# Optimization experiments

Hardware: AMD Instinct MI355X
Metric: run time of the kernel (lower is better)

## Reference

```python
import jax, jax.numpy as jnp
import numpy as np

B, S, E, H, D = 8, 1024, 1024, 16, 64
LN_EPS = 1e-5


def setup_inputs() -> dict:
    key = jax.random.key(0)
    ks = jax.random.split(key, 8)
    scale = 1.0 / np.sqrt(E)
    return {
        "query": jax.random.normal(ks[0], (B, S, E), jnp.float32),
        "key": jax.random.normal(ks[1], (B, S, E), jnp.float32),
        "value": jax.random.normal(ks[2], (B, S, E), jnp.float32),
        "self_attn_mask": jax.random.randint(ks[3], (B, S, S), 0, 2) == 1,
        "Wq": jax.random.normal(ks[4], (E, H * D), jnp.float32) * scale,
        "Wk": jax.random.normal(ks[5], (E, H * D), jnp.float32) * scale,
        "Wv": jax.random.normal(ks[6], (E, H * D), jnp.float32) * scale,
        "Wo": jax.random.normal(ks[7], (H * D, E), jnp.float32) * scale,
        "ln_gamma": jnp.ones((E,), jnp.float32),
        "ln_beta": jnp.zeros((E,), jnp.float32),
    }


def reference(query, key, value, self_attn_mask, Wq, Wk, Wv, Wo, ln_gamma, ln_beta):
    identity = query
    # project and split heads: [B, S, E] -> [B, H, S, D]
    q = (query @ Wq).reshape(B, S, H, D).transpose(0, 2, 1, 3)
    k = (key @ Wk).reshape(B, S, H, D).transpose(0, 2, 1, 3)
    v = (value @ Wv).reshape(B, S, H, D).transpose(0, 2, 1, 3)
    # scaled dot-product scores in fp32, additive mask fill -1e9
    score = jnp.einsum("bhsd,bhtd->bhst", q, k).astype(jnp.float32) / np.sqrt(D)
    score = jnp.where(self_attn_mask[:, None, :, :], jnp.float32(-1e9), score)
    attn = jax.nn.softmax(score, axis=-1)
    degree = jnp.einsum("bhst,bhtd->bhsd", attn, v)  # [B, H, S, D]
    degree = degree.transpose(0, 2, 1, 3).reshape(B, S, H * D)
    out = degree @ Wo + identity
    # LayerNorm over last dim
    mu = jnp.mean(out, axis=-1, keepdims=True)
    var = jnp.var(out, axis=-1, keepdims=True)
    out = (out - mu) * jax.lax.rsqrt(var + LN_EPS) * ln_gamma + ln_beta
    return out
```

## Files before the change

### kernel.cpp

```cpp
#include <hip/hip_runtime.h>
#include <hip/hip_bf16.h>
#include <cstdint>
#include <cstddef>

typedef __attribute__((ext_vector_type(8))) short bf16x8;
typedef __attribute__((ext_vector_type(8))) unsigned short ushort8;
typedef __attribute__((ext_vector_type(4))) unsigned short ushort4v;
typedef __attribute__((ext_vector_type(4))) float f32x4;

#define B_ 8
#define S_ 1024
#define E_ 1024
#define H_ 16
#define D_ 64
#define NW_ (S_ / 64)

__device__ __forceinline__ unsigned short f2bf(float f) {
    union { float fp; unsigned int u; } v; v.fp = f;
    unsigned int u = v.u;
    return (unsigned short)((u + 0x7fffu + ((u >> 16) & 1u)) >> 16);
}

__device__ __forceinline__ float fexp2(float x) {
    return __builtin_amdgcn_exp2f(x);
}

__device__ __forceinline__ unsigned cvt_pk_bf16(float lo, float hi) {
    unsigned r;
    asm("v_cvt_pk_bf16_f32 %0, %1, %2" : "=v"(r) : "v"(lo), "v"(hi));
    return r;
}

__device__ __forceinline__ void gload16(const void* g, void* l) {
    __builtin_amdgcn_global_load_lds((__attribute__((address_space(1))) void*)g,
                                     (__attribute__((address_space(3))) void*)l,
                                     16, 0, 0);
}

__global__ __launch_bounds__(256) void f32_to_bf16(const float* __restrict__ in,
                                                   unsigned short* __restrict__ out,
                                                   int n8) {
    int i = blockIdx.x * 256 + threadIdx.x;
    const int stride = gridDim.x * 256;
    for (; i < n8; i += stride) {
        float4 f0 = ((const float4*)in)[i * 2];
        float4 f1 = ((const float4*)in)[i * 2 + 1];
        union { unsigned u[4]; ushort8 v; } o;
        o.u[0] = cvt_pk_bf16(f0.x, f0.y);
        o.u[1] = cvt_pk_bf16(f0.z, f0.w);
        o.u[2] = cvt_pk_bf16(f1.x, f1.y);
        o.u[3] = cvt_pk_bf16(f1.z, f1.w);
        ((ushort8*)out)[i] = o.v;
    }
}

__global__ __launch_bounds__(256) void wtrans4(const float* __restrict__ W0,
                                               const float* __restrict__ W1,
                                               const float* __restrict__ W2,
                                               const float* __restrict__ W3,
                                               unsigned short* __restrict__ T0,
                                               unsigned short* __restrict__ T1,
                                               unsigned short* __restrict__ T2,
                                               unsigned short* __restrict__ T3) {
    const float* W = (blockIdx.z == 0) ? W0 : (blockIdx.z == 1) ? W1 : (blockIdx.z == 2) ? W2 : W3;
    unsigned short* Wt = (blockIdx.z == 0) ? T0 : (blockIdx.z == 1) ? T1 : (blockIdx.z == 2) ? T2 : T3;
    __shared__ float tile[32][33];
    const int k0 = blockIdx.y * 32, n0 = blockIdx.x * 32;
    const int tx = threadIdx.x & 31, ty = threadIdx.x >> 5;
#pragma unroll
    for (int i = ty; i < 32; i += 8)
        tile[i][tx] = W[(size_t)(k0 + i) * E_ + n0 + tx];
    __syncthreads();
#pragma unroll
    for (int i = ty; i < 32; i += 8)
        Wt[(size_t)(n0 + i) * E_ + k0 + tx] = f2bf(tile[tx][i]);
}

__global__ void detect_kernel(const unsigned int* __restrict__ m, int* __restrict__ flag) {
    unsigned int bad = 0;
    for (int i = threadIdx.x; i < 4096; i += 64) bad |= (m[i] > 1u) ? 1u : 0u;
    unsigned long long anybad = __ballot(bad != 0u);
    if (threadIdx.x == 0) *flag = (anybad == 0ull) ? 1 : 0;
}

__global__ __launch_bounds__(256) void pack_mask(const void* __restrict__ maskp,
                                                 const int* __restrict__ flagp,
                                                 unsigned long long* __restrict__ mbits) {
    const int mask32 = *flagp;
    const int lane = threadIdx.x & 63;
    const int gw = blockIdx.x * 4 + (threadIdx.x >> 6);
    const int nwaves = gridDim.x * 4;
    const int totw = B_ * S_ * NW_;
    for (int w = gw; w < totw; w += nwaves) {
        bool m;
        if (mask32) m = ((const int*)maskp)[(size_t)w * 64 + lane] != 0;
        else        m = ((const unsigned char*)maskp)[(size_t)w * 64 + lane] != 0;
        unsigned long long bits = __ballot(m);
        if (lane == 0) mbits[w] = bits;
    }
}

template <int EPI>
__global__ __launch_bounds__(256) void gemm_bt(const unsigned short* __restrict__ A,
                                               const unsigned short* __restrict__ Bt,
                                               void* __restrict__ Cp,
                                               const float* __restrict__ resid,
                                               float cscale) {
    __shared__ unsigned short As[128 * 64];
    __shared__ unsigned short Bs[128 * 64];
    const int t = threadIdx.x;
    const int lane = t & 63, w = t >> 6;
    const int wr = w >> 1, wc = w & 1;
    const int l15 = lane & 15, l4 = lane >> 4;
    const int m0 = blockIdx.x * 128, n0 = blockIdx.y * 128;

    const int lr = lane >> 3, lc = lane & 7;
    const int csrc = (lc ^ lr) * 8;
    const unsigned short* Ag[4];
    const unsigned short* Bg[4];
#pragma unroll
    for (int g = 0; g < 4; ++g) {
        Ag[g] = A + (size_t)(m0 + w * 32 + g * 8 + lr) * E_ + csrc;
        Bg[g] = Bt + (size_t)(n0 + w * 32 + g * 8 + lr) * E_ + csrc;
    }
    unsigned short* Al = &As[w * 32 * 64];
    unsigned short* Bl = &Bs[w * 32 * 64];

    f32x4 acc[4][4];
#pragma unroll
    for (int i = 0; i < 4; ++i)
#pragma unroll
        for (int j = 0; j < 4; ++j) acc[i][j] = (f32x4){0.f, 0.f, 0.f, 0.f};

    const int r7 = (l15 & 7) << 4;
    const char* AsB = (const char*)As;
    const char* BsB = (const char*)Bs;

    for (int kt = 0; kt < E_; kt += 64) {
#pragma unroll
        for (int g = 0; g < 4; ++g) {
            gload16(Ag[g] + kt, Al + g * 512);
            gload16(Bg[g] + kt, Bl + g * 512);
        }
        __syncthreads();
#pragma unroll
        for (int kk = 0; kk < 2; ++kk) {
            bf16x8 af[4], bfv[4];
#pragma unroll
            for (int mi = 0; mi < 4; ++mi)
                af[mi] = *(const bf16x8*)(AsB + (size_t)(wr * 64 + mi * 16 + l15) * 128 +
                                          ((((kk * 4 + l4) << 4)) ^ r7));
#pragma unroll
            for (int ni = 0; ni < 4; ++ni)
                bfv[ni] = *(const bf16x8*)(BsB + (size_t)(wc * 64 + ni * 16 + l15) * 128 +
                                           ((((kk * 4 + l4) << 4)) ^ r7));
#pragma unroll
            for (int mi = 0; mi < 4; ++mi)
#pragma unroll
                for (int ni = 0; ni < 4; ++ni)
                    acc[mi][ni] = __builtin_amdgcn_mfma_f32_16x16x32_bf16(af[mi], bfv[ni],
                                                                          acc[mi][ni], 0, 0, 0);
        }
        __syncthreads();
    }
#pragma unroll
    for (int mi = 0; mi < 4; ++mi) {
#pragma unroll
        for (int ni = 0; ni < 4; ++ni) {
#pragma unroll
            for (int r = 0; r < 4; ++r) {
                const int m = m0 + wr * 64 + mi * 16 + l4 * 4 + r;
                const int n = n0 + wc * 64 + ni * 16 + l15;
                const float v = acc[mi][ni][r];
                if (EPI == 0) {
                    const int b = m >> 10, s = m & 1023, h = n >> 6, d = n & 63;
                    ((unsigned short*)Cp)[(((size_t)b * H_ + h) * S_ + s) * D_ + d] = f2bf(v * cscale);
                } else if (EPI == 2) {
                    const int b = m >> 10, s = m & 1023, h = n >> 6, d = n & 63;
                    ((unsigned short*)Cp)[(((size_t)b * H_ + h) * D_ + d) * S_ + s] = f2bf(v);
                } else {
                    const size_t idx = (size_t)m * E_ + n;
                    ((float*)Cp)[idx] = v + resid[idx];
                }
            }
        }
    }
}

__global__ __launch_bounds__(256) void attn_kernel(const unsigned short* __restrict__ Qh,
                                                   const unsigned short* __restrict__ Kh,
                                                   const unsigned short* __restrict__ Vt,
                                                   const unsigned long long* __restrict__ mbits,
                                                   unsigned short* __restrict__ degree) {
    __shared__ unsigned short Ks[64 * 64];
    __shared__ unsigned short Vs[64 * 64];
    __shared__ unsigned short Ps[4 * 16 * 64];
    const int t = threadIdx.x;
    const int lane = t & 63, w = t >> 6;
    const int l15 = lane & 15, l4 = lane >> 4;
    const int i = blockIdx.x;
    const int L = (i & 7) * 256 + (i >> 3);
    const int bh = L >> 4, b = bh >> 4, h = bh & 15;
    const int q0 = (L & 15) * 64;
    const int myq = q0 + w * 16 + l15;

    const unsigned long long* mrow = mbits + ((size_t)b * S_ + myq) * NW_;

    bf16x8 qf[2];
    {
        const unsigned short* qptr = Qh + ((size_t)bh * S_ + myq) * D_ + l4 * 8;
        qf[0] = *(const bf16x8*)qptr;
        qf[1] = *(const bf16x8*)(qptr + 32);
    }
    f32x4 O[4];
#pragma unroll
    for (int idx = 0; idx < 4; ++idx) O[idx] = (f32x4){0.f, 0.f, 0.f, 0.f};
    float mrun = -3e38f, lrun = 0.f;

    const int srow = t >> 2, sch = (t & 3) * 2;
    const int ssw = (srow & 7) << 4;
    char* KsB = (char*)Ks;
    char* VsB = (char*)Vs;
    char* PsB = (char*)Ps + w * 2048;
    const int psw = (l15 & 7) << 4;

    const unsigned short* kgb = Kh + ((size_t)bh * S_ + srow) * D_ + sch * 8;
    const unsigned short* vgb = Vt + ((size_t)bh * D_ + srow) * S_ + sch * 8;

    ushort8 kp0 = *(const ushort8*)kgb;
    ushort8 kp1 = *(const ushort8*)(kgb + 8);
    ushort8 vp0 = *(const ushort8*)vgb;
    ushort8 vp1 = *(const ushort8*)(vgb + 8);

    for (int jt = 0; jt < S_; jt += 64) {
        const unsigned long long mw = mrow[jt >> 6];
        *(ushort8*)(KsB + srow * 128 + ((sch * 16) ^ ssw)) = kp0;
        *(ushort8*)(KsB + srow * 128 + ((sch * 16 + 16) ^ ssw)) = kp1;
        *(ushort8*)(VsB + srow * 128 + ((sch * 16) ^ ssw)) = vp0;
        *(ushort8*)(VsB + srow * 128 + ((sch * 16 + 16) ^ ssw)) = vp1;
        if (jt + 64 < S_) {
            kp0 = *(const ushort8*)(kgb + (size_t)(jt + 64) * D_);
            kp1 = *(const ushort8*)(kgb + (size_t)(jt + 64) * D_ + 8);
            vp0 = *(const ushort8*)(vgb + jt + 64);
            vp1 = *(const ushort8*)(vgb + jt + 64 + 8);
        }
        asm volatile("s_waitcnt lgkmcnt(0)" ::: "memory");
        __builtin_amdgcn_s_barrier();

        f32x4 sacc[4];
#pragma unroll
        for (int idx = 0; idx < 4; ++idx) sacc[idx] = (f32x4){0.f, 0.f, 0.f, 0.f};
#pragma unroll
        for (int ni = 0; ni < 4; ++ni) {
            const int row = l15 + ni * 16;
            const int sw = (row & 7) << 4;
            bf16x8 b0 = *(const bf16x8*)(KsB + row * 128 + ((l4 * 16) ^ sw));
            bf16x8 b1 = *(const bf16x8*)(KsB + row * 128 + ((64 + l4 * 16) ^ sw));
            sacc[ni] = __builtin_amdgcn_mfma_f32_16x16x32_bf16(b0, qf[0], sacc[ni], 0, 0, 0);
            sacc[ni] = __builtin_amdgcn_mfma_f32_16x16x32_bf16(b1, qf[1], sacc[ni], 0, 0, 0);
        }

        float gmax[4];
#pragma unroll
        for (int ni = 0; ni < 4; ++ni) {
            const int kbase = ni * 16 + l4 * 4;
            float s0 = ((mw >> (kbase + 0)) & 1ull) ? -1e9f : sacc[ni][0];
            float s1 = ((mw >> (kbase + 1)) & 1ull) ? -1e9f : sacc[ni][1];
            float s2 = ((mw >> (kbase + 2)) & 1ull) ? -1e9f : sacc[ni][2];
            float s3 = ((mw >> (kbase + 3)) & 1ull) ? -1e9f : sacc[ni][3];
            sacc[ni][0] = s0; sacc[ni][1] = s1; sacc[ni][2] = s2; sacc[ni][3] = s3;
            gmax[ni] = fmaxf(fmaxf(s0, s1), fmaxf(s2, s3));
        }
        float m0 = fmaxf(fmaxf(gmax[0], gmax[1]), fmaxf(gmax[2], gmax[3]));
        m0 = fmaxf(m0, __shfl_xor(m0, 16, 64));
        m0 = fmaxf(m0, __shfl_xor(m0, 32, 64));
        if (!__all(m0 <= mrun + 8.f)) {
            const float mnew = fmaxf(mrun, m0);
            const float corr = fexp2(mrun - mnew);
            lrun *= corr;
#pragma unroll
            for (int df = 0; df < 4; ++df)
#pragma unroll
                for (int r = 0; r < 4; ++r) O[df][r] *= corr;
            mrun = mnew;
        }
        float psn[4];
#pragma unroll
        for (int ni = 0; ni < 4; ++ni) {
            float p0 = fexp2(sacc[ni][0] - mrun);
            float p1 = fexp2(sacc[ni][1] - mrun);
            float p2 = fexp2(sacc[ni][2] - mrun);
            float p3 = fexp2(sacc[ni][3] - mrun);
            psn[ni] = (p0 + p1) + (p2 + p3);
            uint2 pw;
            pw.x = cvt_pk_bf16(p0, p1);
            pw.y = cvt_pk_bf16(p2, p3);
            *(uint2*)(PsB + l15 * 128 + ((ni * 32 + l4 * 8) ^ psw)) = pw;
        }
        float ps = (psn[0] + psn[1]) + (psn[2] + psn[3]);
        ps += __shfl_xor(ps, 16, 64);
        ps += __shfl_xor(ps, 32, 64);
        lrun += ps;

        asm volatile("s_waitcnt lgkmcnt(0)" ::: "memory");
        bf16x8 pa0 = *(const bf16x8*)(PsB + l15 * 128 + ((l4 * 16) ^ psw));
        bf16x8 pa1 = *(const bf16x8*)(PsB + l15 * 128 + ((64 + l4 * 16) ^ psw));
#pragma unroll
        for (int df = 0; df < 4; ++df) {
            const int row = l15 + df * 16;
            const int sw = (row & 7) << 4;
            bf16x8 v0 = *(const bf16x8*)(VsB + row * 128 + ((l4 * 16) ^ sw));
            bf16x8 v1 = *(const bf16x8*)(VsB + row * 128 + ((64 + l4 * 16) ^ sw));
            O[df] = __builtin_amdgcn_mfma_f32_16x16x32_bf16(v0, pa0, O[df], 0, 0, 0);
            O[df] = __builtin_amdgcn_mfma_f32_16x16x32_bf16(v1, pa1, O[df], 0, 0, 0);
        }
        __builtin_amdgcn_s_barrier();
    }

    const float inv = 1.f / lrun;
#pragma unroll
    for (int df = 0; df < 4; ++df) {
        ushort4v ow;
#pragma unroll
        for (int r = 0; r < 4; ++r) ow[r] = f2bf(O[df][r] * inv);
        const size_t dst = ((size_t)b * S_ + myq) * (size_t)(H_ * D_) +
                           h * 64 + df * 16 + l4 * 4;
        *(ushort4v*)(degree + dst) = ow;
    }
}

__global__ __launch_bounds__(256) void lnorm(float* __restrict__ io,
                                             const float* __restrict__ gamma,
                                             const float* __restrict__ beta) {
    const int row = blockIdx.x;
    const int t = threadIdx.x;
    float4 v = ((const float4*)(io + (size_t)row * E_))[t];
    float s = v.x + v.y + v.z + v.w;
    float q = v.x * v.x + v.y * v.y + v.z * v.z + v.w * v.w;
#pragma unroll
    for (int off = 32; off; off >>= 1) {
        s += __shfl_down(s, off, 64);
        q += __shfl_down(q, off, 64);
    }
    __shared__ float red[8];
    const int wid = t >> 6;
    if ((t & 63) == 0) { red[wid] = s; red[4 + wid] = q; }
    __syncthreads();
    const float ts = red[0] + red[1] + red[2] + red[3];
    const float tq = red[4] + red[5] + red[6] + red[7];
    const float mean = ts * (1.0f / E_);
    const float var = tq * (1.0f / E_) - mean * mean;
    const float rstd = rsqrtf(var + 1e-5f);
    const float4 g = ((const float4*)gamma)[t];
    const float4 bb = ((const float4*)beta)[t];
    v.x = (v.x - mean) * rstd * g.x + bb.x;
    v.y = (v.y - mean) * rstd * g.y + bb.y;
    v.z = (v.z - mean) * rstd * g.z + bb.z;
    v.w = (v.w - mean) * rstd * g.w + bb.w;
    ((float4*)(io + (size_t)row * E_))[t] = v;
}

extern "C" void kernel_launch(void* const* d_in, const int* in_sizes, int n_in,
                              void* d_out, int out_size, void* d_ws, size_t ws_size,
                              hipStream_t stream) {
    const float* query = (const float*)d_in[0];
    const float* key_ = (const float*)d_in[1];
    const float* value = (const float*)d_in[2];
    const void* maskp = d_in[3];
    const float* Wq = (const float*)d_in[4];
    const float* Wk = (const float*)d_in[5];
    const float* Wv = (const float*)d_in[6];
    const float* Wo = (const float*)d_in[7];
    const float* gamma = (const float*)d_in[8];
    const float* beta = (const float*)d_in[9];
    float* out = (float*)d_out;
    char* ws = (char*)d_ws;
    const size_t MB = 1024ull * 1024ull;

    unsigned short* WqT = (unsigned short*)(ws + 0 * MB);
    unsigned short* WkT = (unsigned short*)(ws + 2 * MB);
    unsigned short* WvT = (unsigned short*)(ws + 4 * MB);
    unsigned short* WoT = (unsigned short*)(ws + 6 * MB);
    unsigned short* Qh = (unsigned short*)(ws + 8 * MB);
    unsigned short* Kh = (unsigned short*)(ws + 24 * MB);
    unsigned short* Vt = (unsigned short*)(ws + 40 * MB);
    unsigned short* deg = (unsigned short*)(ws + 56 * MB);
    unsigned short* Abf = deg;
    int* flag = (int*)(ws + 72 * MB);
    unsigned long long* mbits = (unsigned long long*)(ws + 72 * MB + 4096);

    const int n8 = B_ * S_ * E_ / 8;
    const float qscale = 0.125f * 1.4426950408889634f;

    wtrans4<<<dim3(32, 32, 4), 256, 0, stream>>>(Wq, Wk, Wv, Wo, WqT, WkT, WvT, WoT);
    detect_kernel<<<1, 64, 0, stream>>>((const unsigned int*)maskp, flag);
    pack_mask<<<2048, 256, 0, stream>>>(maskp, flag, mbits);

    f32_to_bf16<<<2048, 256, 0, stream>>>(query, Abf, n8);
    gemm_bt<0><<<dim3(64, 8), 256, 0, stream>>>(Abf, WqT, Qh, nullptr, qscale);
    f32_to_bf16<<<2048, 256, 0, stream>>>(key_, Abf, n8);
    gemm_bt<0><<<dim3(64, 8), 256, 0, stream>>>(Abf, WkT, Kh, nullptr, 1.0f);
    f32_to_bf16<<<2048, 256, 0, stream>>>(value, Abf, n8);
    gemm_bt<2><<<dim3(64, 8), 256, 0, stream>>>(Abf, WvT, Vt, nullptr, 1.0f);

    attn_kernel<<<2048, 256, 0, stream>>>(Qh, Kh, Vt, mbits, deg);

    gemm_bt<3><<<dim3(64, 8), 256, 0, stream>>>(deg, WoT, out, query, 1.0f);
    lnorm<<<8192, 256, 0, stream>>>(out, gamma, beta);
}
```

Baseline: 246.9 us.

## Raise attention occupancy by aliasing P buffer onto K tile and dropping prefetch

The attention kernel now declares a minimum of 8 blocks per CU, removes the separate P shared-memory buffer by reusing the K tile region after an added barrier, and drops the register prefetch of the next K/V tile in favor of direct loads at loop start. The goal is to cut shared-memory and register use so more waves stay resident and hide latency. The cost is an extra barrier per iteration and the loss of explicit global-load/compute overlap within a block.

```diff
diff --git a/kernel.cpp b/kernel.cpp
--- a/kernel.cpp
+++ b/kernel.cpp
@@ -187,14 +187,13 @@
     }
 }
 
-__global__ __launch_bounds__(256) void attn_kernel(const unsigned short* __restrict__ Qh,
-                                                   const unsigned short* __restrict__ Kh,
-                                                   const unsigned short* __restrict__ Vt,
-                                                   const unsigned long long* __restrict__ mbits,
-                                                   unsigned short* __restrict__ degree) {
+__global__ __launch_bounds__(256, 8) void attn_kernel(const unsigned short* __restrict__ Qh,
+                                                      const unsigned short* __restrict__ Kh,
+                                                      const unsigned short* __restrict__ Vt,
+                                                      const unsigned long long* __restrict__ mbits,
+                                                      unsigned short* __restrict__ degree) {
     __shared__ unsigned short Ks[64 * 64];
     __shared__ unsigned short Vs[64 * 64];
-    __shared__ unsigned short Ps[4 * 16 * 64];
     const int t = threadIdx.x;
     const int lane = t & 63, w = t >> 6;
     const int l15 = lane & 15, l4 = lane >> 4;
@@ -221,31 +220,20 @@
     const int ssw = (srow & 7) << 4;
     char* KsB = (char*)Ks;
     char* VsB = (char*)Vs;
-    char* PsB = (char*)Ps + w * 2048;
+    char* PsB = (char*)Ks + w * 2048;
     const int psw = (l15 & 7) << 4;
 
-    const unsigned short* kgb = Kh + ((size_t)bh * S_ + srow) * D_ + sch * 8;
-    const unsigned short* vgb = Vt + ((size_t)bh * D_ + srow) * S_ + sch * 8;
-
-    ushort8 kp0 = *(const ushort8*)kgb;
-    ushort8 kp1 = *(const ushort8*)(kgb + 8);
-    ushort8 vp0 = *(const ushort8*)vgb;
-    ushort8 vp1 = *(const ushort8*)(vgb + 8);
-
     for (int jt = 0; jt < S_; jt += 64) {
+        {
+            const unsigned short* kg = Kh + ((size_t)bh * S_ + jt + srow) * D_ + sch * 8;
+            *(ushort8*)(KsB + srow * 128 + ((sch * 16) ^ ssw)) = *(const ushort8*)kg;
+            *(ushort8*)(KsB + srow * 128 + ((sch * 16 + 16) ^ ssw)) = *(const ushort8*)(kg + 8);
+            const unsigned short* vg = Vt + ((size_t)bh * D_ + srow) * S_ + jt + sch * 8;
+            *(ushort8*)(VsB + srow * 128 + ((sch * 16) ^ ssw)) = *(const ushort8*)vg;
+            *(ushort8*)(VsB + srow * 128 + ((sch * 16 + 16) ^ ssw)) = *(const ushort8*)(vg + 8);
+        }
         const unsigned long long mw = mrow[jt >> 6];
-        *(ushort8*)(KsB + srow * 128 + ((sch * 16) ^ ssw)) = kp0;
-        *(ushort8*)(KsB + srow * 128 + ((sch * 16 + 16) ^ ssw)) = kp1;
-        *(ushort8*)(VsB + srow * 128 + ((sch * 16) ^ ssw)) = vp0;
-        *(ushort8*)(VsB + srow * 128 + ((sch * 16 + 16) ^ ssw)) = vp1;
-        if (jt + 64 < S_) {
-            kp0 = *(const ushort8*)(kgb + (size_t)(jt + 64) * D_);
-            kp1 = *(const ushort8*)(kgb + (size_t)(jt + 64) * D_ + 8);
-            vp0 = *(const ushort8*)(vgb + jt + 64);
-            vp1 = *(const ushort8*)(vgb + jt + 64 + 8);
-        }
-        asm volatile("s_waitcnt lgkmcnt(0)" ::: "memory");
-        __builtin_amdgcn_s_barrier();
+        __syncthreads();
 
         f32x4 sacc[4];
 #pragma unroll
@@ -259,19 +247,19 @@
             sacc[ni] = __builtin_amdgcn_mfma_f32_16x16x32_bf16(b0, qf[0], sacc[ni], 0, 0, 0);
             sacc[ni] = __builtin_amdgcn_mfma_f32_16x16x32_bf16(b1, qf[1], sacc[ni], 0, 0, 0);
         }
-
-        float gmax[4];
+        __syncthreads();
+
+        float m0 = -3e38f;
 #pragma unroll
         for (int ni = 0; ni < 4; ++ni) {
-            const int kbase = ni * 16 + l4 * 4;
-            float s0 = ((mw >> (kbase + 0)) & 1ull) ? -1e9f : sacc[ni][0];
-            float s1 = ((mw >> (kbase + 1)) & 1ull) ? -1e9f : sacc[ni][1];
-            float s2 = ((mw >> (kbase + 2)) & 1ull) ? -1e9f : sacc[ni][2];
-            float s3 = ((mw >> (kbase + 3)) & 1ull) ? -1e9f : sacc[ni][3];
-            sacc[ni][0] = s0; sacc[ni][1] = s1; sacc[ni][2] = s2; sacc[ni][3] = s3;
-            gmax[ni] = fmaxf(fmaxf(s0, s1), fmaxf(s2, s3));
-        }
-        float m0 = fmaxf(fmaxf(gmax[0], gmax[1]), fmaxf(gmax[2], gmax[3]));
+#pragma unroll
+            for (int r = 0; r < 4; ++r) {
+                const int k = ni * 16 + l4 * 4 + r;
+                const float s = ((mw >> k) & 1ull) ? -1e9f : sacc[ni][r];
+                sacc[ni][r] = s;
+                m0 = fmaxf(m0, s);
+            }
+        }
         m0 = fmaxf(m0, __shfl_xor(m0, 16, 64));
         m0 = fmaxf(m0, __shfl_xor(m0, 32, 64));
         if (!__all(m0 <= mrun + 8.f)) {
@@ -284,20 +272,19 @@
                 for (int r = 0; r < 4; ++r) O[df][r] *= corr;
             mrun = mnew;
         }
-        float psn[4];
+        float ps = 0.f;
 #pragma unroll
         for (int ni = 0; ni < 4; ++ni) {
             float p0 = fexp2(sacc[ni][0] - mrun);
             float p1 = fexp2(sacc[ni][1] - mrun);
             float p2 = fexp2(sacc[ni][2] - mrun);
             float p3 = fexp2(sacc[ni][3] - mrun);
-            psn[ni] = (p0 + p1) + (p2 + p3);
+            ps += (p0 + p1) + (p2 + p3);
             uint2 pw;
             pw.x = cvt_pk_bf16(p0, p1);
             pw.y = cvt_pk_bf16(p2, p3);
             *(uint2*)(PsB + l15 * 128 + ((ni * 32 + l4 * 8) ^ psw)) = pw;
         }
-        float ps = (psn[0] + psn[1]) + (psn[2] + psn[3]);
         ps += __shfl_xor(ps, 16, 64);
         ps += __shfl_xor(ps, 32, 64);
         lrun += ps;
@@ -314,7 +301,7 @@
             O[df] = __builtin_amdgcn_mfma_f32_16x16x32_bf16(v0, pa0, O[df], 0, 0, 0);
             O[df] = __builtin_amdgcn_mfma_f32_16x16x32_bf16(v1, pa1, O[df], 0, 0, 0);
         }
-        __builtin_amdgcn_s_barrier();
+        __syncthreads();
     }
 
     const float inv = 1.f / lrun;
```

New measurement: 405.5 us. 1.64x slower.
